# Kernel optimization log

Measured on AMD Instinct MI355X. Metric: run time of the kernel, lower is better.

## Reference

```python
import jax, jax.numpy as jnp
import numpy as np

N_NODES = 50000
N_EDGES = 1_600_000
D_IN = 128
D_HID = 128
N_CLASSES = 8
N_GRAPHS = 64


def setup_inputs() -> dict:
    key = jax.random.key(0)
    ks = jax.random.split(key, 8)
    x = jax.random.normal(ks[0], (N_NODES, D_IN), dtype=jnp.float32)
    edge_index = jax.random.randint(ks[1], (2, N_EDGES), 0, N_NODES, dtype=jnp.int32)
    graph_ids = jnp.sort(jax.random.randint(ks[2], (N_NODES,), 0, N_GRAPHS, dtype=jnp.int32))
    s = 1.0 / np.sqrt(D_HID)
    W1 = jax.random.normal(ks[3], (D_IN, D_HID), dtype=jnp.float32) * s
    b1 = jnp.zeros((D_HID,), dtype=jnp.float32)
    W2 = jax.random.normal(ks[4], (D_HID, D_HID), dtype=jnp.float32) * s
    b2 = jnp.zeros((D_HID,), dtype=jnp.float32)
    Wc = jax.random.normal(ks[5], (D_HID, N_CLASSES), dtype=jnp.float32) * s
    bc = jnp.zeros((N_CLASSES,), dtype=jnp.float32)
    return {"x": x, "edge_index": edge_index, "graph_ids": graph_ids,
            "W1": W1, "b1": b1, "W2": W2, "b2": b2, "Wc": Wc, "bc": bc}


def _gcn_layer(h, src, dst, norm, W, b):
    # message: gather source features, apply symmetric degree normalization
    msg = h[src] * norm[:, None]                       # [E, d]
    agg = jax.ops.segment_sum(msg, dst, num_segments=N_NODES)  # [N, d]
    return jax.nn.relu(agg @ W + b)


def reference(x, edge_index, graph_ids, W1, b1, W2, b2, Wc, bc):
    src, dst = edge_index[0], edge_index[1]
    ones_e = jnp.ones((N_EDGES,), dtype=x.dtype)
    deg = jax.ops.segment_sum(ones_e, dst, num_segments=N_NODES)
    deg_inv_sqrt = jnp.where(deg > 0, jax.lax.rsqrt(jnp.maximum(deg, 1.0)), 0.0)
    norm = deg_inv_sqrt[src] * deg_inv_sqrt[dst]       # [E]

    h = _gcn_layer(x, src, dst, norm, W1, b1)
    h = _gcn_layer(h, src, dst, norm, W2, b2)

    # per-graph mean pooling (segment mean over nodes of each graph)
    ones_n = jnp.ones((N_NODES,), dtype=h.dtype)
    counts = jax.ops.segment_sum(ones_n, graph_ids, num_segments=N_GRAPHS)
    pooled = jax.ops.segment_sum(h, graph_ids, num_segments=N_GRAPHS)
    pooled = pooled / jnp.maximum(counts, 1.0)[:, None]  # [G, d]

    logits = pooled @ Wc + bc                           # [G, n_classes]
    return logits
```

## Files before the change

### kernel.cpp

```cpp
#include <hip/hip_runtime.h>
#include <hip/hip_bf16.h>

#define D_HID 128
#define N_GRAPHS 64
#define N_CLASSES 8
#define NPB 16
#define CAP 96


__device__ inline unsigned short f2b(float x) {
    unsigned int u = __float_as_uint(x);
    unsigned int r = (u + 0x7fffu + ((u >> 16) & 1u)) >> 16;
    return (unsigned short)r;
}
__device__ inline float b2f(unsigned short u) {
    return __uint_as_float((unsigned int)u << 16);
}

__global__ __launch_bounds__(256) void prep_kernel(const float* __restrict__ x,
                                                   uint2* __restrict__ xb4,
                                                   int castBlocks, int n4,
                                                   const int* __restrict__ src,
                                                   const int* __restrict__ dst,
                                                   int* __restrict__ cursor,
                                                   unsigned short* __restrict__ csr16,
                                                   int E, int N) {
    const int b = blockIdx.x;
    if (b < castBlocks) {
        int i = b * 256 + threadIdx.x;
        if (i < n4) {
            float4 v = ((const float4*)x)[i];
            uint2 o;
            o.x = (unsigned int)f2b(v.x) | ((unsigned int)f2b(v.y) << 16);
            o.y = (unsigned int)f2b(v.z) | ((unsigned int)f2b(v.w) << 16);
            xb4[i] = o;
        }
        return;
    }
    const int e = (b - castBlocks) * 256 + threadIdx.x;
    if (e >= E) return;
    const int d = dst[e];
    const int s = src[e];
    const int slot = atomicAdd(&cursor[d], 1);
    if (slot < CAP) csr16[(size_t)d * CAP + slot] = (unsigned short)s;
}

__global__ __launch_bounds__(256) void dis_counts_kernel(const int* __restrict__ deg,
                                                         float* __restrict__ dis,
                                                         const int* __restrict__ gid,
                                                         int* __restrict__ counts, int N) {
    int n = blockIdx.x * blockDim.x + threadIdx.x;
    if (n < N) {
        int v = deg[n];
        dis[n] = (v > 0) ? rsqrtf((float)v) : 0.0f;
    }
    if (blockIdx.x == 0 && threadIdx.x < N_GRAPHS) {
        int g = threadIdx.x;
        int lo0 = 0, hi0 = N;
        while (lo0 < hi0) { int mid = (lo0 + hi0) >> 1; if (gid[mid] < g) lo0 = mid + 1; else hi0 = mid; }
        int lo1 = lo0, hi1 = N;
        while (lo1 < hi1) { int mid = (lo1 + hi1) >> 1; if (gid[mid] < g + 1) lo1 = mid + 1; else hi1 = mid; }
        counts[g] = lo1 - lo0;
    }
}

__global__ __launch_bounds__(256) void layer_kernel(const unsigned short* __restrict__ h_in,
                                                    const int* __restrict__ deg,
                                                    const unsigned short* __restrict__ csr16,
                                                    const float* __restrict__ dis,
                                                    const float* __restrict__ W,
                                                    const float* __restrict__ bias,
                                                    unsigned short* __restrict__ h_out,
                                                    float* __restrict__ pooled,
                                                    const int* __restrict__ gid,
                                                    int fuse_pool, int N) {
    const int base = blockIdx.x * NPB;
    const int tid = threadIdx.x;
    const int wv = tid >> 6;
    const int lane = tid & 63;
    const int q = lane >> 4;
    const int ql = lane & 15;
    __shared__ float s_agg[NPB][D_HID];

    const int n0 = base + wv * 4;
    float acc[4][8] = {};
    int dd[4];
    #pragma unroll
    for (int i = 0; i < 4; ++i) {
        const int n = n0 + i;
        dd[i] = (n < N) ? min(deg[n], CAP) : 0;
    }
    const int dm = max(max(dd[0], dd[1]), max(dd[2], dd[3]));

    for (int cb = 0; cb < dm; cb += 64) {
        const int cm = min(64, dm - cb);
        unsigned int pk[4];
        #pragma unroll
        for (int i = 0; i < 4; ++i) {
            pk[i] = 0u;
            if (lane < dd[i] - cb) {
                unsigned int u = (unsigned int)csr16[(size_t)(n0 + i) * CAP + cb + lane];
                pk[i] = u | ((unsigned int)f2b(dis[u]) << 16);
            }
        }
        #pragma unroll 4
        for (int j = 0; j < cm; j += 4) {
            const int e = j + q;
            #pragma unroll
            for (int i = 0; i < 4; ++i) {
                const unsigned int p = (unsigned int)__shfl((int)pk[i], e);
                const float w = __uint_as_float(p & 0xffff0000u);
                const uint4 r = *(const uint4*)&h_in[(size_t)(p & 0xffffu) * D_HID + ql * 8];
                acc[i][0] = fmaf(w, __uint_as_float(r.x << 16), acc[i][0]);
                acc[i][1] = fmaf(w, __uint_as_float(r.x & 0xffff0000u), acc[i][1]);
                acc[i][2] = fmaf(w, __uint_as_float(r.y << 16), acc[i][2]);
                acc[i][3] = fmaf(w, __uint_as_float(r.y & 0xffff0000u), acc[i][3]);
                acc[i][4] = fmaf(w, __uint_as_float(r.z << 16), acc[i][4]);
                acc[i][5] = fmaf(w, __uint_as_float(r.z & 0xffff0000u), acc[i][5]);
                acc[i][6] = fmaf(w, __uint_as_float(r.w << 16), acc[i][6]);
                acc[i][7] = fmaf(w, __uint_as_float(r.w & 0xffff0000u), acc[i][7]);
            }
        }
    }

    #pragma unroll
    for (int i = 0; i < 4; ++i) {
        #pragma unroll
        for (int k = 0; k < 8; ++k) {
            acc[i][k] += __shfl_down(acc[i][k], 32);
            acc[i][k] += __shfl_down(acc[i][k], 16);
        }
        if (q == 0) {
            const float dn = (n0 + i < N) ? dis[n0 + i] : 0.0f;
            #pragma unroll
            for (int k = 0; k < 8; ++k) s_agg[wv * 4 + i][ql * 8 + k] = acc[i][k] * dn;
        }
    }
    __syncthreads();

    const int t = tid & 127;
    const int nb = tid >> 7;
    float outv[8];
    const float bt = bias[t];
    #pragma unroll
    for (int i = 0; i < 8; ++i) outv[i] = bt;

    for (int k = 0; k < D_HID; k += 4) {
        const float w0 = W[(k + 0) * D_HID + t];
        const float w1 = W[(k + 1) * D_HID + t];
        const float w2 = W[(k + 2) * D_HID + t];
        const float w3 = W[(k + 3) * D_HID + t];
        #pragma unroll
        for (int i = 0; i < 8; ++i) {
            float4 a = *(const float4*)&s_agg[nb * 8 + i][k];
            outv[i] = fmaf(a.x, w0, outv[i]);
            outv[i] = fmaf(a.y, w1, outv[i]);
            outv[i] = fmaf(a.z, w2, outv[i]);
            outv[i] = fmaf(a.w, w3, outv[i]);
        }
    }

    #pragma unroll
    for (int i = 0; i < 8; ++i) {
        const int n = base + nb * 8 + i;
        if (n >= N) break;
        float v = fmaxf(outv[i], 0.0f);
        if (fuse_pool) {
            atomicAdd(&pooled[gid[n] * D_HID + t], v);
        } else {
            h_out[(size_t)n * D_HID + t] = f2b(v);
        }
    }
}

__global__ __launch_bounds__(128) void pool_kernel(const unsigned short* __restrict__ h,
                                                   const int* __restrict__ gid,
                                                   float* __restrict__ pooled,
                                                   int N, int nodes_per_block) {
    const int t = threadIdx.x;
    const int start = blockIdx.x * nodes_per_block;
    if (start >= N) return;
    const int endn = min(start + nodes_per_block, N);
    int cur = gid[start];
    float sum = 0.0f;
    for (int n = start; n < endn; ++n) {
        int g = gid[n];
        if (g != cur) {
            atomicAdd(&pooled[cur * D_HID + t], sum);
            cur = g; sum = 0.0f;
        }
        sum += b2f(h[(size_t)n * D_HID + t]);
    }
    atomicAdd(&pooled[cur * D_HID + t], sum);
}

__global__ __launch_bounds__(512) void classify_kernel(const float* __restrict__ pooled,
                                                       const int* __restrict__ counts,
                                                       const float* __restrict__ Wc,
                                                       const float* __restrict__ bc,
                                                       float* __restrict__ out) {
    const int g = threadIdx.x >> 3;
    const int c = threadIdx.x & 7;
    float inv = 1.0f / fmaxf((float)counts[g], 1.0f);
    float acc = bc[c];
    #pragma unroll 8
    for (int k = 0; k < D_HID; ++k) {
        acc = fmaf(pooled[g * D_HID + k] * inv, Wc[k * N_CLASSES + c], acc);
    }
    out[g * N_CLASSES + c] = acc;
}

extern "C" void kernel_launch(void* const* d_in, const int* in_sizes, int n_in,
                              void* d_out, int out_size, void* d_ws, size_t ws_size,
                              hipStream_t stream) {
    const float* x   = (const float*)d_in[0];
    const int* edge  = (const int*)d_in[1];
    const int* gid   = (const int*)d_in[2];
    const float* W1  = (const float*)d_in[3];
    const float* b1  = (const float*)d_in[4];
    const float* W2  = (const float*)d_in[5];
    const float* b2  = (const float*)d_in[6];
    const float* Wc  = (const float*)d_in[7];
    const float* bc  = (const float*)d_in[8];
    float* out       = (float*)d_out;

    const int E = in_sizes[1] / 2;
    const int N = in_sizes[2];
    const int* src = edge;
    const int* dst = edge + E;

    char* p = (char*)d_ws;
    auto take = [&](size_t bytes) {
        char* r = p;
        p += (bytes + 255) & ~(size_t)255;
        return r;
    };
    int*   cursor  = (int*)take((size_t)N * 4);
    float* dis     = (float*)take((size_t)N * 4);
    float* pooled  = (float*)take((size_t)N_GRAPHS * D_HID * 4);
    int*   counts  = (int*)take((size_t)N_GRAPHS * 4);
    unsigned short* csr16 = (unsigned short*)take((size_t)N * CAP * 2);
    unsigned short* xb  = (unsigned short*)take((size_t)N * D_HID * 2);
    unsigned short* h1b = (unsigned short*)take((size_t)N * D_HID * 2);
    size_t used = (size_t)(p - (char*)d_ws);
    size_t h2_bytes = (size_t)N * D_HID * 2;
    const bool separate_pool = (used + h2_bytes <= ws_size);
    unsigned short* h2b = separate_pool ? (unsigned short*)take(h2_bytes) : nullptr;

    hipMemsetAsync(cursor, 0, (size_t)N * 4, stream);
    hipMemsetAsync(pooled, 0, (size_t)N_GRAPHS * D_HID * 4, stream);

    const int EB = 256;
    const int n4 = (N * D_HID) / 4;
    const int castBlocks = (n4 + EB - 1) / EB;
    const int fillBlocks = (E + EB - 1) / EB;
    prep_kernel<<<castBlocks + fillBlocks, EB, 0, stream>>>(
        x, (uint2*)xb, castBlocks, n4, src, dst, cursor, csr16, E, N);
    dis_counts_kernel<<<(N + EB - 1) / EB, EB, 0, stream>>>(cursor, dis, gid, counts, N);

    const int LG = (N + NPB - 1) / NPB;
    layer_kernel<<<LG, 256, 0, stream>>>(xb, cursor, csr16, dis, W1, b1, h1b, pooled, gid, 0, N);

    if (separate_pool) {
        layer_kernel<<<LG, 256, 0, stream>>>(h1b, cursor, csr16, dis, W2, b2, h2b, pooled, gid, 0, N);
        const int NPBLK = 8;
        pool_kernel<<<(N + NPBLK - 1) / NPBLK, 128, 0, stream>>>(h2b, gid, pooled, N, NPBLK);
    } else {
        layer_kernel<<<LG, 256, 0, stream>>>(h1b, cursor, csr16, dis, W2, b2, nullptr, pooled, gid, 1, N);
    }

    classify_kernel<<<1, 512, 0, stream>>>(pooled, counts, Wc, bc, out);
}
```

Before: 408.5 us.

## Partition CSR fill by destination range per XCD with vectorized edge loads

The edge-fill pass is split into 8 partitions, one per XCD, chosen by block index mod 8 to match round-robin block dispatch. Each block handles only edges whose destination falls in its partition's node range, so atomics on a given cursor entry and the matching CSR writes come from a single XCD and stay in its L2. Edge indices are also loaded four at a time as int4. In exchange, every partition rereads the full src/dst arrays, which multiplies edge-index traffic by eight and launches eight times as many fill blocks.

```diff
diff --git a/kernel.cpp b/kernel.cpp
--- a/kernel.cpp
+++ b/kernel.cpp
@@ -6,6 +6,7 @@
 #define N_CLASSES 8
 #define NPB 16
 #define CAP 96
+#define NXCD 8
 
 
 __device__ inline unsigned short f2b(float x) {
@@ -24,7 +25,8 @@
                                                    const int* __restrict__ dst,
                                                    int* __restrict__ cursor,
                                                    unsigned short* __restrict__ csr16,
-                                                   int E, int N) {
+                                                   int E, int N, int fillBlocks,
+                                                   int dstRange) {
     const int b = blockIdx.x;
     if (b < castBlocks) {
         int i = b * 256 + threadIdx.x;
@@ -37,12 +39,31 @@
         }
         return;
     }
-    const int e = (b - castBlocks) * 256 + threadIdx.x;
-    if (e >= E) return;
-    const int d = dst[e];
-    const int s = src[e];
-    const int slot = atomicAdd(&cursor[d], 1);
-    if (slot < CAP) csr16[(size_t)d * CAP + slot] = (unsigned short)s;
+    const int fb = b - castBlocks;
+    const int chunk = fb >> 3;
+    const int part  = b & 7;
+    const int t = chunk * 256 + threadIdx.x;
+    const int e0 = t * 4;
+    if (e0 >= E) return;
+    const int dlo = part * dstRange;
+    if (e0 + 3 < E) {
+        const int4 d4 = ((const int4*)dst)[t];
+        const int4 s4 = ((const int4*)src)[t];
+        #pragma unroll
+        for (int k = 0; k < 4; ++k) {
+            const int d = (&d4.x)[k];
+            if ((unsigned)(d - dlo) >= (unsigned)dstRange) continue;
+            const int slot = atomicAdd(&cursor[d], 1);
+            if (slot < CAP) csr16[(size_t)d * CAP + slot] = (unsigned short)(&s4.x)[k];
+        }
+    } else {
+        for (int k = 0; e0 + k < E; ++k) {
+            const int d = dst[e0 + k];
+            if ((unsigned)(d - dlo) >= (unsigned)dstRange) continue;
+            const int slot = atomicAdd(&cursor[d], 1);
+            if (slot < CAP) csr16[(size_t)d * CAP + slot] = (unsigned short)src[e0 + k];
+        }
+    }
 }
 
 __global__ __launch_bounds__(256) void dis_counts_kernel(const int* __restrict__ deg,
@@ -253,9 +274,10 @@
     const int EB = 256;
     const int n4 = (N * D_HID) / 4;
     const int castBlocks = (n4 + EB - 1) / EB;
-    const int fillBlocks = (E + EB - 1) / EB;
-    prep_kernel<<<castBlocks + fillBlocks, EB, 0, stream>>>(
-        x, (uint2*)xb, castBlocks, n4, src, dst, cursor, csr16, E, N);
+    const int fillBlocks = ((E + 3) / 4 + EB - 1) / EB;
+    const int dstRange = (N + NXCD - 1) / NXCD;
+    prep_kernel<<<castBlocks + NXCD * fillBlocks, EB, 0, stream>>>(
+        x, (uint2*)xb, castBlocks, n4, src, dst, cursor, csr16, E, N, fillBlocks, dstRange);
     dis_counts_kernel<<<(N + EB - 1) / EB, EB, 0, stream>>>(cursor, dis, gid, counts, N);
 
     const int LG = (N + NPB - 1) / NPB;
```

Result: faster. 356.4 us (-12.8%).
